# Kernel optimization log

Measured on AMD Instinct MI355X. Metric: run time of the kernel, lower is better.

Reference implementation:

```python
import jax, jax.numpy as jnp
import numpy as np

N_NODES = 50000

def _gcn_layer(x, src, dst, W, b, n_nodes):
    # Linear transform first (PyG GCNConv): h = x @ W
    h = x @ W  # [N, out]
    # Add self-loops
    loop = jnp.arange(n_nodes, dtype=src.dtype)
    src2 = jnp.concatenate([src, loop])
    dst2 = jnp.concatenate([dst, loop])
    # Symmetric normalization deg^-1/2 (deg counts incoming edges incl. self-loop)
    deg = jax.ops.segment_sum(jnp.ones_like(dst2, dtype=h.dtype), dst2, num_segments=n_nodes)
    dinv = jnp.where(deg > 0, jax.lax.rsqrt(deg), 0.0)
    norm = dinv[src2] * dinv[dst2]  # [E+N]
    # Gather-scale-scatter aggregation
    msg = h[src2] * norm[:, None]  # [E+N, out]
    out = jax.ops.segment_sum(msg, dst2, num_segments=n_nodes)
    return out + b

def setup_inputs() -> dict:
    key = jax.random.key(0)
    k1, k2, k3, k4 = jax.random.split(key, 4)
    E = 800000
    x = jax.random.normal(k1, (N_NODES, 128), dtype=jnp.float32)
    edge_index = jax.random.randint(k2, (2, E), 0, N_NODES, dtype=jnp.int64)
    W1 = jax.random.normal(k3, (128, 512), dtype=jnp.float32) * (1.0 / np.sqrt(128))
    b1 = jnp.zeros((512,), dtype=jnp.float32)
    W2 = jax.random.normal(k4, (512, 250), dtype=jnp.float32) * (1.0 / np.sqrt(512))
    b2 = jnp.zeros((250,), dtype=jnp.float32)
    return {"x": x, "edge_index": edge_index, "W1": W1, "b1": b1, "W2": W2, "b2": b2}

def reference(x, edge_index, W1, b1, W2, b2):
    src, dst = edge_index[0], edge_index[1]
    h = _gcn_layer(x, src, dst, W1, b1, N_NODES)
    h = jax.nn.relu(h)
    h = _gcn_layer(h, src, dst, W2, b2, N_NODES)
    return jax.nn.relu(h)
```

## Files before the change

### kernel.cpp

```cpp
#include <hip/hip_runtime.h>

#define N_NODES 50000

typedef __attribute__((ext_vector_type(8))) short bf16x8;
typedef __attribute__((ext_vector_type(4))) float f32x4;

__device__ __forceinline__ ushort f2bf(float f) {
    union { float f; unsigned u; } v; v.f = f;
    unsigned r = v.u + 0x7fff + ((v.u >> 16) & 1);
    return (ushort)(r >> 16);
}
__device__ __forceinline__ float bf2f(ushort u) {
    union { unsigned u; float f; } v; v.u = ((unsigned)u) << 16;
    return v.f;
}
__device__ __forceinline__ float bf2f_lo(unsigned u) {
    union { unsigned u; float f; } v; v.u = u << 16;
    return v.f;
}
__device__ __forceinline__ float bf2f_hi(unsigned u) {
    union { unsigned u; float f; } v; v.u = u & 0xffff0000u;
    return v.f;
}

__device__ __forceinline__ int eload(const void* ei, int idx, int is64) {
    return is64 ? (int)((const long long*)ei)[idx] : ((const int*)ei)[idx];
}

__global__ void k_init(const void* ei, int* flag, int* deg, int n) {
    if (blockIdx.x == 0) {
        __shared__ int bad;
        if (threadIdx.x == 0) bad = 0;
        __syncthreads();
        long long v = ((const long long*)ei)[threadIdx.x];
        if (v < 0 || v >= N_NODES) atomicOr(&bad, 1);
        __syncthreads();
        if (threadIdx.x == 0) *flag = bad ? 0 : 1;
    }
    int i = blockIdx.x * 256 + threadIdx.x;
    if (i < n) deg[i] = 0;
}

__global__ void k_hist(const void* ei, const int* flag, int* deg, int e) {
    int base = (blockIdx.x * blockDim.x + threadIdx.x) * 4;
    if (base >= e) return;
    int is64 = *flag;
    if (base + 4 <= e) {
        int d0 = eload(ei, e + base,     is64);
        int d1 = eload(ei, e + base + 1, is64);
        int d2 = eload(ei, e + base + 2, is64);
        int d3 = eload(ei, e + base + 3, is64);
        atomicAdd(&deg[d0], 1);
        atomicAdd(&deg[d1], 1);
        atomicAdd(&deg[d2], 1);
        atomicAdd(&deg[d3], 1);
    } else {
        for (int i = base; i < e; ++i)
            atomicAdd(&deg[eload(ei, e + i, is64)], 1);
    }
}

__global__ __launch_bounds__(512)
void k_scanA(const int* __restrict__ deg, int* __restrict__ rp1,
             int* __restrict__ bsum, int n) {
    __shared__ int wsum[8];
    const int i = blockIdx.x * 512 + threadIdx.x;
    const int lane = threadIdx.x & 63, wid = threadIdx.x >> 6;
    int x = (i < n) ? deg[i] : 0;
    #pragma unroll
    for (int off = 1; off < 64; off <<= 1) {
        int y = __shfl_up(x, off, 64);
        if (lane >= off) x += y;
    }
    if (lane == 63) wsum[wid] = x;
    __syncthreads();
    if (wid == 0 && lane < 8) {
        int s = wsum[lane];
        #pragma unroll
        for (int off = 1; off < 8; off <<= 1) {
            int y = __shfl_up(s, off, 64);
            if (lane >= off) s += y;
        }
        wsum[lane] = s;
    }
    __syncthreads();
    int incl = x + (wid > 0 ? wsum[wid - 1] : 0);
    if (i < n) rp1[i] = incl;
    if (threadIdx.x == 0) bsum[blockIdx.x] = wsum[7];
}

__global__ __launch_bounds__(512)
void k_scanC(const int* __restrict__ deg, int* __restrict__ rowptr,
             const int* __restrict__ bsum, int* __restrict__ cur,
             float* __restrict__ dinv, int n, int nb) {
    __shared__ int spart[2];
    if (threadIdx.x < 128) {
        int v = (threadIdx.x < nb && (int)threadIdx.x < (int)blockIdx.x)
                ? bsum[threadIdx.x] : 0;
        #pragma unroll
        for (int o = 32; o; o >>= 1) v += __shfl_down(v, o, 64);
        if ((threadIdx.x & 63) == 0) spart[threadIdx.x >> 6] = v;
    }
    __syncthreads();
    const int off = spart[0] + spart[1];
    const int i = blockIdx.x * 512 + threadIdx.x;
    if (i >= n) return;
    const int d = deg[i];
    const int incl = rowptr[i + 1] + off;
    rowptr[i + 1] = incl;
    cur[i] = incl - d;
    dinv[i] = rsqrtf((float)(d + 1));
    if (i == 0) rowptr[0] = 0;
}

__global__ void k_fill(const void* ei, const int* flag, int* cur, int* adj, int e) {
    const int phase = blockIdx.x & 7;
    const int lo = phase * (N_NODES / 8);
    const int hi = lo + (N_NODES / 8);
    const int i = (blockIdx.x >> 3) * 256 + threadIdx.x;
    if (i >= e) return;
    const int is64 = *flag;
    const int d = eload(ei, e + i, is64);
    if (d >= lo && d < hi) {
        const int s = eload(ei, i, is64);
        adj[atomicAdd(&cur[d], 1)] = s;
    }
}

__global__ void k_splitW(const float* __restrict__ W1, const float* __restrict__ W2,
                         ushort* __restrict__ o1, ushort* __restrict__ o2) {
    int idx = blockIdx.x * 256 + threadIdx.x;
    if (idx < 512 * 128) {
        int nn = idx >> 7, k = idx & 127;
        o1[idx] = f2bf(W1[(size_t)k * 512 + nn]);
    } else {
        idx -= 512 * 128;
        int nn = idx >> 9, k = idx & 511;
        o2[idx] = (nn < 250) ? f2bf(W2[(size_t)k * 250 + nn]) : (ushort)0;
    }
}

__global__ __launch_bounds__(256)
void k_scale(const float* __restrict__ x, const float* __restrict__ dinv,
             ushort* __restrict__ xs, int n) {
    int idx = blockIdx.x * 256 + threadIdx.x;
    if (idx >= n * 64) return;
    int i = idx >> 6;
    float2 v = ((const float2*)x)[idx];
    float d = dinv[i];
    ((unsigned*)xs)[idx] = (unsigned)f2bf(d * v.x) | ((unsigned)f2bf(d * v.y) << 16);
}

__global__ __launch_bounds__(256)
void k_pull128b(const int* __restrict__ rowptr, const int* __restrict__ adj,
                const float* __restrict__ dinv, const ushort* __restrict__ xs,
                ushort* __restrict__ ohi, int n) {
    const int i = blockIdx.x * 4 + (threadIdx.x >> 6);
    if (i >= n) return;
    const int lane = threadIdx.x & 63;
    const unsigned* xs32 = (const unsigned*)xs;
    unsigned u = xs32[(size_t)i * 64 + lane];
    float a0 = bf2f_lo(u), a1 = bf2f_hi(u);
    int j = rowptr[i];
    const int end = rowptr[i + 1];
    for (; j + 8 <= end; j += 8) {
        int s0 = adj[j],     s1 = adj[j + 1], s2 = adj[j + 2], s3 = adj[j + 3];
        int s4 = adj[j + 4], s5 = adj[j + 5], s6 = adj[j + 6], s7 = adj[j + 7];
        unsigned u0 = xs32[(size_t)s0 * 64 + lane];
        unsigned u1 = xs32[(size_t)s1 * 64 + lane];
        unsigned u2 = xs32[(size_t)s2 * 64 + lane];
        unsigned u3 = xs32[(size_t)s3 * 64 + lane];
        unsigned u4 = xs32[(size_t)s4 * 64 + lane];
        unsigned u5 = xs32[(size_t)s5 * 64 + lane];
        unsigned u6 = xs32[(size_t)s6 * 64 + lane];
        unsigned u7 = xs32[(size_t)s7 * 64 + lane];
        a0 += bf2f_lo(u0) + bf2f_lo(u1) + bf2f_lo(u2) + bf2f_lo(u3);
        a1 += bf2f_hi(u0) + bf2f_hi(u1) + bf2f_hi(u2) + bf2f_hi(u3);
        a0 += bf2f_lo(u4) + bf2f_lo(u5) + bf2f_lo(u6) + bf2f_lo(u7);
        a1 += bf2f_hi(u4) + bf2f_hi(u5) + bf2f_hi(u6) + bf2f_hi(u7);
    }
    for (; j + 4 <= end; j += 4) {
        int s0 = adj[j], s1 = adj[j + 1], s2 = adj[j + 2], s3 = adj[j + 3];
        unsigned u0 = xs32[(size_t)s0 * 64 + lane];
        unsigned u1 = xs32[(size_t)s1 * 64 + lane];
        unsigned u2 = xs32[(size_t)s2 * 64 + lane];
        unsigned u3 = xs32[(size_t)s3 * 64 + lane];
        a0 += bf2f_lo(u0) + bf2f_lo(u1) + bf2f_lo(u2) + bf2f_lo(u3);
        a1 += bf2f_hi(u0) + bf2f_hi(u1) + bf2f_hi(u2) + bf2f_hi(u3);
    }
    for (; j < end; ++j) {
        unsigned us = xs32[(size_t)adj[j] * 64 + lane];
        a0 += bf2f_lo(us);
        a1 += bf2f_hi(us);
    }
    const float di = dinv[i];
    a0 *= di; a1 *= di;
    ((unsigned*)ohi)[(size_t)i * 64 + lane] =
        (unsigned)f2bf(a0) | ((unsigned)f2bf(a1) << 16);
}

__global__ __launch_bounds__(256)
void k_pull250v(const int* __restrict__ rowptr, const int* __restrict__ adj,
                const float* __restrict__ dinv, const ushort* __restrict__ t,
                const float* __restrict__ bias, float* __restrict__ out, int n) {
    const int i = blockIdx.x * 4 + (threadIdx.x >> 6);
    if (i >= n) return;
    const int lane = threadIdx.x & 63;
    const uint2* t2 = (const uint2*)t;
    uint2 u = t2[(size_t)i * 64 + lane];
    float a0 = bf2f_lo(u.x), a1 = bf2f_hi(u.x);
    float a2 = bf2f_lo(u.y), a3 = bf2f_hi(u.y);
    int j = rowptr[i];
    const int end = rowptr[i + 1];
    for (; j + 8 <= end; j += 8) {
        int s0 = adj[j],     s1 = adj[j + 1], s2 = adj[j + 2], s3 = adj[j + 3];
        int s4 = adj[j + 4], s5 = adj[j + 5], s6 = adj[j + 6], s7 = adj[j + 7];
        uint2 u0 = t2[(size_t)s0 * 64 + lane];
        uint2 u1 = t2[(size_t)s1 * 64 + lane];
        uint2 u2 = t2[(size_t)s2 * 64 + lane];
        uint2 u3 = t2[(size_t)s3 * 64 + lane];
        uint2 u4 = t2[(size_t)s4 * 64 + lane];
        uint2 u5 = t2[(size_t)s5 * 64 + lane];
        uint2 u6 = t2[(size_t)s6 * 64 + lane];
        uint2 u7 = t2[(size_t)s7 * 64 + lane];
        a0 += bf2f_lo(u0.x) + bf2f_lo(u1.x) + bf2f_lo(u2.x) + bf2f_lo(u3.x);
        a1 += bf2f_hi(u0.x) + bf2f_hi(u1.x) + bf2f_hi(u2.x) + bf2f_hi(u3.x);
        a2 += bf2f_lo(u0.y) + bf2f_lo(u1.y) + bf2f_lo(u2.y) + bf2f_lo(u3.y);
        a3 += bf2f_hi(u0.y) + bf2f_hi(u1.y) + bf2f_hi(u2.y) + bf2f_hi(u3.y);
        a0 += bf2f_lo(u4.x) + bf2f_lo(u5.x) + bf2f_lo(u6.x) + bf2f_lo(u7.x);
        a1 += bf2f_hi(u4.x) + bf2f_hi(u5.x) + bf2f_hi(u6.x) + bf2f_hi(u7.x);
        a2 += bf2f_lo(u4.y) + bf2f_lo(u5.y) + bf2f_lo(u6.y) + bf2f_lo(u7.y);
        a3 += bf2f_hi(u4.y) + bf2f_hi(u5.y) + bf2f_hi(u6.y) + bf2f_hi(u7.y);
    }
    for (; j + 4 <= end; j += 4) {
        int s0 = adj[j], s1 = adj[j + 1], s2 = adj[j + 2], s3 = adj[j + 3];
        uint2 u0 = t2[(size_t)s0 * 64 + lane];
        uint2 u1 = t2[(size_t)s1 * 64 + lane];
        uint2 u2 = t2[(size_t)s2 * 64 + lane];
        uint2 u3 = t2[(size_t)s3 * 64 + lane];
        a0 += bf2f_lo(u0.x) + bf2f_lo(u1.x) + bf2f_lo(u2.x) + bf2f_lo(u3.x);
        a1 += bf2f_hi(u0.x) + bf2f_hi(u1.x) + bf2f_hi(u2.x) + bf2f_hi(u3.x);
        a2 += bf2f_lo(u0.y) + bf2f_lo(u1.y) + bf2f_lo(u2.y) + bf2f_lo(u3.y);
        a3 += bf2f_hi(u0.y) + bf2f_hi(u1.y) + bf2f_hi(u2.y) + bf2f_hi(u3.y);
    }
    for (; j < end; ++j) {
        uint2 us = t2[(size_t)adj[j] * 64 + lane];
        a0 += bf2f_lo(us.x); a1 += bf2f_hi(us.x);
        a2 += bf2f_lo(us.y); a3 += bf2f_hi(us.y);
    }
    const float d = dinv[i];
    const int c0 = lane * 4;
    if (lane < 62) {
        float2 b0 = *(const float2*)&bias[c0];
        float2 b1 = *(const float2*)&bias[c0 + 2];
        float2 o0, o1;
        o0.x = fmaxf(d * a0 + b0.x, 0.0f);
        o0.y = fmaxf(d * a1 + b0.y, 0.0f);
        o1.x = fmaxf(d * a2 + b1.x, 0.0f);
        o1.y = fmaxf(d * a3 + b1.y, 0.0f);
        *(float2*)&out[(size_t)i * 250 + c0] = o0;
        *(float2*)&out[(size_t)i * 250 + c0 + 2] = o1;
    } else if (lane == 62) {
        float2 b0 = *(const float2*)&bias[248];
        float2 o0;
        o0.x = fmaxf(d * a0 + b0.x, 0.0f);
        o0.y = fmaxf(d * a1 + b0.y, 0.0f);
        *(float2*)&out[(size_t)i * 250 + 248] = o0;
    }
}

__device__ __forceinline__ void gl16(const ushort* g, ushort* l) {
    __builtin_amdgcn_global_load_lds((const __attribute__((address_space(1))) void*)g,
                                     (__attribute__((address_space(3))) void*)l,
                                     16, 0, 0);
}

#define OFF_B 4096
#define SMEM_HALF 8192

__global__ __launch_bounds__(256, 3)
void k_mfma(const ushort* __restrict__ A, const ushort* __restrict__ B,
            const float* __restrict__ bias, const float* __restrict__ rscale,
            ushort* __restrict__ outp, int M, int K, int ldc, int mode,
            int CX, int PY) {
    __shared__ __align__(16) ushort smem[2 * SMEM_HALF];

    int id = blockIdx.x;
    const int gsz = CX * 8;
    const int nfull = (PY >> 3) * gsz;
    int bx, by;
    if (id < nfull) {
        int gg = id / gsz;
        int r  = id - gg * gsz;
        bx = r >> 3;
        by = gg * 8 + (r & 7);
    } else {
        int rem  = id - nfull;
        int pbase = (PY >> 3) << 3;
        int prem  = PY - pbase;
        by = pbase + rem % prem;
        bx = rem / prem;
    }
    const int brow = by * 128;
    const int bcol = bx * 128;

    const int tid  = threadIdx.x;
    const int lane = tid & 63;
    const int w    = tid >> 6;
    const int g    = lane >> 4;
    const int lr   = lane & 15;
    const int wm   = w >> 1, wn = w & 1;

    auto STAGE = [&](ushort* buf, int k0) {
        #pragma unroll
        for (int t2 = 0; t2 < 2; ++t2) {
            const int b  = w * 2 + t2;
            const int c  = b >> 1;
            const int r0 = (b & 1) * 64;
            const int kofs = k0 + c * 8;
            const int doff = c * 1024 + r0 * 8;
            gl16(A + (size_t)(brow + r0 + lane) * K + kofs, buf + doff);
            gl16(B + (size_t)(bcol + r0 + lane) * K + kofs, buf + OFF_B + doff);
        }
    };

    f32x4 acc[4][4] = {};

    auto COMPUTE = [&](const ushort* rb) {
        bf16x8 af[4], bh[4];
        #pragma unroll
        for (int i = 0; i < 4; ++i) {
            af[i] = *(const bf16x8*)(rb + g * 1024 + (wm * 64 + i * 16 + lr) * 8);
            bh[i] = *(const bf16x8*)(rb + OFF_B + g * 1024 + (wn * 64 + i * 16 + lr) * 8);
        }
        #pragma unroll
        for (int mt = 0; mt < 4; ++mt)
            #pragma unroll
            for (int nt = 0; nt < 4; ++nt)
                acc[mt][nt] = __builtin_amdgcn_mfma_f32_16x16x32_bf16(bh[nt], af[mt], acc[mt][nt], 0, 0, 0);
    };

    STAGE(smem, 0);
    int cur = 0;
    for (int k0 = 32; k0 < K; k0 += 32) {
        STAGE(smem + (cur ^ 1) * SMEM_HALF, k0);
        asm volatile("s_waitcnt vmcnt(4)" ::: "memory");
        __builtin_amdgcn_sched_barrier(0);
        __builtin_amdgcn_s_barrier();
        COMPUTE(smem + cur * SMEM_HALF);
        __builtin_amdgcn_sched_barrier(0);
        __builtin_amdgcn_s_barrier();
        cur ^= 1;
    }
    asm volatile("s_waitcnt vmcnt(0)" ::: "memory");
    __builtin_amdgcn_sched_barrier(0);
    __builtin_amdgcn_s_barrier();
    COMPUTE(smem + cur * SMEM_HALF);

    #pragma unroll
    for (int mt = 0; mt < 4; ++mt) {
        const int gr = brow + wm * 64 + mt * 16 + lr;
        if (gr >= M) continue;
        const float rs = (mode == 0) ? rscale[gr] : 0.0f;
        #pragma unroll
        for (int nt = 0; nt < 4; ++nt) {
            const int gc0 = bcol + wn * 64 + nt * 16 + g * 4;
            float v0, v1, v2, v3;
            if (mode == 0) {
                v0 = acc[mt][nt][0] * rs; v1 = acc[mt][nt][1] * rs;
                v2 = acc[mt][nt][2] * rs; v3 = acc[mt][nt][3] * rs;
            } else {
                const float4 bv = *(const float4*)&bias[gc0];
                v0 = fmaxf(acc[mt][nt][0] + bv.x, 0.0f);
                v1 = fmaxf(acc[mt][nt][1] + bv.y, 0.0f);
                v2 = fmaxf(acc[mt][nt][2] + bv.z, 0.0f);
                v3 = fmaxf(acc[mt][nt][3] + bv.w, 0.0f);
            }
            uint2 pk;
            pk.x = (unsigned)f2bf(v0) | ((unsigned)f2bf(v1) << 16);
            pk.y = (unsigned)f2bf(v2) | ((unsigned)f2bf(v3) << 16);
            *(uint2*)(outp + (size_t)gr * ldc + gc0) = pk;
        }
    }
}

extern "C" void kernel_launch(void* const* d_in, const int* in_sizes, int n_in,
                              void* d_out, int out_size, void* d_ws, size_t ws_size,
                              hipStream_t stream) {
    const float* x  = (const float*)d_in[0];
    const void*  ei = d_in[1];
    const float* W1 = (const float*)d_in[2];
    const float* b1 = (const float*)d_in[3];
    const float* W2 = (const float*)d_in[4];
    const float* b2 = (const float*)d_in[5];
    float* out = (float*)d_out;

    const int N = N_NODES;
    const int E = in_sizes[1] / 2;
    const int MPAD = 50048;
    const int NSCB = (N + 511) / 512;

    char* base = (char*)d_ws;
    int*   flag   = (int*)base;
    int*   deg    = (int*)(base + 256);
    int*   rowptr = deg + 51200;
    int*   cur    = rowptr + 51200;
    float* dinv   = (float*)(cur + 51200);
    int*   bsum   = (int*)(dinv + 51200);
    int*   adj    = bsum + 128;
    char*  p      = (char*)(adj + ((E + 63) & ~63));
    ushort* A1hi  = (ushort*)p;  p += (size_t)MPAD * 128 * 2;
    ushort* A1xx  = (ushort*)p;  p += (size_t)MPAD * 128 * 2;
    ushort* tbuf  = A1hi;
    ushort* h1hi  = (ushort*)p;  p += (size_t)MPAD * 512 * 2;
    ushort* Bt1   = (ushort*)p;  p += 512 * 128 * 2;
    ushort* Bt2   = (ushort*)p;  p += 256 * 512 * 2;
    ushort* xs    = (ushort*)p;  p += (size_t)MPAD * 128 * 2;
    (void)A1xx;

    k_init<<<(N + 255) / 256, 256, 0, stream>>>(ei, flag, deg, N);
    k_hist<<<(E / 4 + 255) / 256, 256, 0, stream>>>(ei, flag, deg, E);
    k_scanA<<<NSCB, 512, 0, stream>>>(deg, rowptr + 1, bsum, N);
    k_scanC<<<NSCB, 512, 0, stream>>>(deg, rowptr, bsum, cur, dinv, N, NSCB);
    k_fill<<<((E + 255) / 256) * 8, 256, 0, stream>>>(ei, flag, cur, adj, E);

    k_splitW<<<(512 * 128 + 256 * 512) / 256, 256, 0, stream>>>(W1, W2, Bt1, Bt2);
    k_scale<<<(N * 64 + 255) / 256, 256, 0, stream>>>(x, dinv, xs, N);

    k_pull128b<<<(N + 3) / 4, 256, 0, stream>>>(rowptr, adj, dinv, xs, A1hi, N);

    k_mfma<<<4 * 391, 256, 0, stream>>>(A1hi, Bt1, b1, nullptr, h1hi,
                                        N, 128, 512, 1, 4, 391);

    k_mfma<<<2 * 391, 256, 0, stream>>>(h1hi, Bt2, nullptr, dinv, tbuf,
                                        N, 512, 256, 0, 2, 391);

    k_pull250v<<<(N + 3) / 4, 256, 0, stream>>>(rowptr, adj, dinv, tbuf, b2, out, N);
}
```

Before: 266.8 us.

## Fuse both dense GEMMs into one kernel keeping hidden layer in LDS

Replaces the two separate MFMA GEMM launches with a single kernel. Each 64-row block computes the 512-wide hidden activations (bias+ReLU, bf16) into shared memory, then immediately multiplies by W2 and scales by dinv. This removes the global write and re-read of the 50k×512 hidden tensor and one launch. In exchange it drops the LDS double-buffered staging and loads operands directly from global memory. The large LDS footprint (about 66KB per block) also limits occupancy.

```diff
diff --git a/kernel.cpp b/kernel.cpp
--- a/kernel.cpp
+++ b/kernel.cpp
@@ -269,117 +269,101 @@
     }
 }
 
-__device__ __forceinline__ void gl16(const ushort* g, ushort* l) {
-    __builtin_amdgcn_global_load_lds((const __attribute__((address_space(1))) void*)g,
-                                     (__attribute__((address_space(3))) void*)l,
-                                     16, 0, 0);
-}
-
-#define OFF_B 4096
-#define SMEM_HALF 8192
-
-__global__ __launch_bounds__(256, 3)
-void k_mfma(const ushort* __restrict__ A, const ushort* __restrict__ B,
-            const float* __restrict__ bias, const float* __restrict__ rscale,
-            ushort* __restrict__ outp, int M, int K, int ldc, int mode,
-            int CX, int PY) {
-    __shared__ __align__(16) ushort smem[2 * SMEM_HALF];
-
-    int id = blockIdx.x;
-    const int gsz = CX * 8;
-    const int nfull = (PY >> 3) * gsz;
-    int bx, by;
-    if (id < nfull) {
-        int gg = id / gsz;
-        int r  = id - gg * gsz;
-        bx = r >> 3;
-        by = gg * 8 + (r & 7);
-    } else {
-        int rem  = id - nfull;
-        int pbase = (PY >> 3) << 3;
-        int prem  = PY - pbase;
-        by = pbase + rem % prem;
-        bx = rem / prem;
-    }
-    const int brow = by * 128;
-    const int bcol = bx * 128;
-
+#define H1PAD 520
+
+__global__ __launch_bounds__(512, 4)
+void k_fused(const ushort* __restrict__ A1, const ushort* __restrict__ Bt1,
+             const ushort* __restrict__ Bt2, const float* __restrict__ b1,
+             const float* __restrict__ dinv, ushort* __restrict__ t, int M) {
+    __shared__ __align__(16) ushort h1s[64 * H1PAD];
     const int tid  = threadIdx.x;
     const int lane = tid & 63;
     const int w    = tid >> 6;
     const int g    = lane >> 4;
     const int lr   = lane & 15;
-    const int wm   = w >> 1, wn = w & 1;
-
-    auto STAGE = [&](ushort* buf, int k0) {
-        #pragma unroll
-        for (int t2 = 0; t2 < 2; ++t2) {
-            const int b  = w * 2 + t2;
-            const int c  = b >> 1;
-            const int r0 = (b & 1) * 64;
-            const int kofs = k0 + c * 8;
-            const int doff = c * 1024 + r0 * 8;
-            gl16(A + (size_t)(brow + r0 + lane) * K + kofs, buf + doff);
-            gl16(B + (size_t)(bcol + r0 + lane) * K + kofs, buf + OFF_B + doff);
+    const int brow = blockIdx.x * 64;
+
+    #pragma unroll
+    for (int half = 0; half < 2; ++half) {
+        f32x4 acc[4][2] = {};
+        const ushort* aB[4];
+        const ushort* bB[2];
+        #pragma unroll
+        for (int mt = 0; mt < 4; ++mt)
+            aB[mt] = A1 + (size_t)(brow + mt * 16 + lr) * 128 + g * 8;
+        #pragma unroll
+        for (int nt = 0; nt < 2; ++nt)
+            bB[nt] = Bt1 + (size_t)(w * 64 + half * 32 + nt * 16 + lr) * 128 + g * 8;
+        #pragma unroll
+        for (int kk = 0; kk < 128; kk += 32) {
+            bf16x8 af[4], bh[2];
+            #pragma unroll
+            for (int mt = 0; mt < 4; ++mt) af[mt] = *(const bf16x8*)(aB[mt] + kk);
+            #pragma unroll
+            for (int nt = 0; nt < 2; ++nt) bh[nt] = *(const bf16x8*)(bB[nt] + kk);
+            #pragma unroll
+            for (int mt = 0; mt < 4; ++mt)
+                #pragma unroll
+                for (int nt = 0; nt < 2; ++nt)
+                    acc[mt][nt] = __builtin_amdgcn_mfma_f32_16x16x32_bf16(bh[nt], af[mt], acc[mt][nt], 0, 0, 0);
         }
-    };
-
-    f32x4 acc[4][4] = {};
-
-    auto COMPUTE = [&](const ushort* rb) {
-        bf16x8 af[4], bh[4];
-        #pragma unroll
-        for (int i = 0; i < 4; ++i) {
-            af[i] = *(const bf16x8*)(rb + g * 1024 + (wm * 64 + i * 16 + lr) * 8);
-            bh[i] = *(const bf16x8*)(rb + OFF_B + g * 1024 + (wn * 64 + i * 16 + lr) * 8);
+        #pragma unroll
+        for (int mt = 0; mt < 4; ++mt) {
+            const int r = mt * 16 + lr;
+            #pragma unroll
+            for (int nt = 0; nt < 2; ++nt) {
+                const int c0 = w * 64 + half * 32 + nt * 16 + g * 4;
+                const float4 bv = *(const float4*)&b1[c0];
+                float v0 = fmaxf(acc[mt][nt][0] + bv.x, 0.0f);
+                float v1 = fmaxf(acc[mt][nt][1] + bv.y, 0.0f);
+                float v2 = fmaxf(acc[mt][nt][2] + bv.z, 0.0f);
+                float v3 = fmaxf(acc[mt][nt][3] + bv.w, 0.0f);
+                uint2 pk;
+                pk.x = (unsigned)f2bf(v0) | ((unsigned)f2bf(v1) << 16);
+                pk.y = (unsigned)f2bf(v2) | ((unsigned)f2bf(v3) << 16);
+                *(uint2*)&h1s[r * H1PAD + c0] = pk;
+            }
         }
+    }
+    __syncthreads();
+
+    {
+        f32x4 acc[4][2] = {};
+        const ushort* lB[4];
+        const ushort* bB[2];
         #pragma unroll
         for (int mt = 0; mt < 4; ++mt)
-            #pragma unroll
-            for (int nt = 0; nt < 4; ++nt)
-                acc[mt][nt] = __builtin_amdgcn_mfma_f32_16x16x32_bf16(bh[nt], af[mt], acc[mt][nt], 0, 0, 0);
-    };
-
-    STAGE(smem, 0);
-    int cur = 0;
-    for (int k0 = 32; k0 < K; k0 += 32) {
-        STAGE(smem + (cur ^ 1) * SMEM_HALF, k0);
-        asm volatile("s_waitcnt vmcnt(4)" ::: "memory");
-        __builtin_amdgcn_sched_barrier(0);
-        __builtin_amdgcn_s_barrier();
-        COMPUTE(smem + cur * SMEM_HALF);
-        __builtin_amdgcn_sched_barrier(0);
-        __builtin_amdgcn_s_barrier();
-        cur ^= 1;
-    }
-    asm volatile("s_waitcnt vmcnt(0)" ::: "memory");
-    __builtin_amdgcn_sched_barrier(0);
-    __builtin_amdgcn_s_barrier();
-    COMPUTE(smem + cur * SMEM_HALF);
-
-    #pragma unroll
-    for (int mt = 0; mt < 4; ++mt) {
-        const int gr = brow + wm * 64 + mt * 16 + lr;
-        if (gr >= M) continue;
-        const float rs = (mode == 0) ? rscale[gr] : 0.0f;
-        #pragma unroll
-        for (int nt = 0; nt < 4; ++nt) {
-            const int gc0 = bcol + wn * 64 + nt * 16 + g * 4;
-            float v0, v1, v2, v3;
-            if (mode == 0) {
-                v0 = acc[mt][nt][0] * rs; v1 = acc[mt][nt][1] * rs;
-                v2 = acc[mt][nt][2] * rs; v3 = acc[mt][nt][3] * rs;
-            } else {
-                const float4 bv = *(const float4*)&bias[gc0];
-                v0 = fmaxf(acc[mt][nt][0] + bv.x, 0.0f);
-                v1 = fmaxf(acc[mt][nt][1] + bv.y, 0.0f);
-                v2 = fmaxf(acc[mt][nt][2] + bv.z, 0.0f);
-                v3 = fmaxf(acc[mt][nt][3] + bv.w, 0.0f);
+            lB[mt] = h1s + (mt * 16 + lr) * H1PAD + g * 8;
+        #pragma unroll
+        for (int nt = 0; nt < 2; ++nt)
+            bB[nt] = Bt2 + (size_t)(w * 32 + nt * 16 + lr) * 512 + g * 8;
+        #pragma unroll 4
+        for (int kk = 0; kk < 512; kk += 32) {
+            bf16x8 af[4], bh[2];
+            #pragma unroll
+            for (int mt = 0; mt < 4; ++mt) af[mt] = *(const bf16x8*)(lB[mt] + kk);
+            #pragma unroll
+            for (int nt = 0; nt < 2; ++nt) bh[nt] = *(const bf16x8*)(bB[nt] + kk);
+            #pragma unroll
+            for (int mt = 0; mt < 4; ++mt)
+                #pragma unroll
+                for (int nt = 0; nt < 2; ++nt)
+                    acc[mt][nt] = __builtin_amdgcn_mfma_f32_16x16x32_bf16(bh[nt], af[mt], acc[mt][nt], 0, 0, 0);
+        }
+        #pragma unroll
+        for (int mt = 0; mt < 4; ++mt) {
+            const int gr = brow + mt * 16 + lr;
+            const float rs = dinv[gr];
+            #pragma unroll
+            for (int nt = 0; nt < 2; ++nt) {
+                const int c0 = w * 32 + nt * 16 + g * 4;
+                uint2 pk;
+                pk.x = (unsigned)f2bf(acc[mt][nt][0] * rs) |
+                       ((unsigned)f2bf(acc[mt][nt][1] * rs) << 16);
+                pk.y = (unsigned)f2bf(acc[mt][nt][2] * rs) |
+                       ((unsigned)f2bf(acc[mt][nt][3] * rs) << 16);
+                *(uint2*)&t[(size_t)gr * 256 + c0] = pk;
             }
-            uint2 pk;
-            pk.x = (unsigned)f2bf(v0) | ((unsigned)f2bf(v1) << 16);
-            pk.y = (unsigned)f2bf(v2) | ((unsigned)f2bf(v3) << 16);
-            *(uint2*)(outp + (size_t)gr * ldc + gc0) = pk;
         }
     }
 }
@@ -410,13 +394,10 @@
     int*   adj    = bsum + 128;
     char*  p      = (char*)(adj + ((E + 63) & ~63));
     ushort* A1hi  = (ushort*)p;  p += (size_t)MPAD * 128 * 2;
-    ushort* A1xx  = (ushort*)p;  p += (size_t)MPAD * 128 * 2;
-    ushort* tbuf  = A1hi;
-    ushort* h1hi  = (ushort*)p;  p += (size_t)MPAD * 512 * 2;
+    ushort* tbuf  = (ushort*)p;  p += (size_t)MPAD * 256 * 2;
     ushort* Bt1   = (ushort*)p;  p += 512 * 128 * 2;
     ushort* Bt2   = (ushort*)p;  p += 256 * 512 * 2;
     ushort* xs    = (ushort*)p;  p += (size_t)MPAD * 128 * 2;
-    (void)A1xx;
 
     k_init<<<(N + 255) / 256, 256, 0, stream>>>(ei, flag, deg, N);
     k_hist<<<(E / 4 + 255) / 256, 256, 0, stream>>>(ei, flag, deg, E);
@@ -429,11 +410,7 @@
 
     k_pull128b<<<(N + 3) / 4, 256, 0, stream>>>(rowptr, adj, dinv, xs, A1hi, N);
 
-    k_mfma<<<4 * 391, 256, 0, stream>>>(A1hi, Bt1, b1, nullptr, h1hi,
-                                        N, 128, 512, 1, 4, 391);
-
-    k_mfma<<<2 * 391, 256, 0, stream>>>(h1hi, Bt2, nullptr, dinv, tbuf,
-                                        N, 512, 256, 0, 2, 391);
+    k_fused<<<MPAD / 64, 512, 0, stream>>>(A1hi, Bt1, Bt2, b1, dinv, tbuf, N);
 
     k_pull250v<<<(N + 3) / 4, 256, 0, stream>>>(rowptr, adj, dinv, tbuf, b2, out, N);
 }
```

Result: slower. 277.3 us (+3.9%).
